# Optimization experiments

Measured on AMD Instinct MI355X. Metric: run time of the kernel, lower is better.

The kernel has to match this reference:

```python
import jax, jax.numpy as jnp
import numpy as np

NEG_SLOPE = 0.2


def add_self_loops(edge_index, num_nodes):
    loop = jnp.arange(num_nodes, dtype=edge_index.dtype)
    return jnp.concatenate([edge_index, jnp.stack([loop, loop])], axis=1)


def gat_conv(x, edge_index, W, att_src, att_dst, bias, heads, out_ch, concat):
    # x: [N, F_in]; edge_index: [2, E]; W: [F_in, heads*out_ch]
    # att_src/att_dst: [heads, out_ch]; bias: [heads*out_ch] or [out_ch]
    N = x.shape[0]
    ei = add_self_loops(edge_index, N)
    src, dst = ei[0], ei[1]
    xw = (x @ W).reshape(N, heads, out_ch)          # [N, H, C]
    a_src = jnp.einsum('nhc,hc->nh', xw, att_src)    # [N, H]
    a_dst = jnp.einsum('nhc,hc->nh', xw, att_dst)    # [N, H]
    e = a_src[src] + a_dst[dst]                      # [E', H]
    e = jax.nn.leaky_relu(e, NEG_SLOPE)
    # segment softmax over edges grouped by destination node
    e_max = jax.ops.segment_max(e, dst, num_segments=N)  # [N, H]
    e_exp = jnp.exp(e - e_max[dst])
    denom = jax.ops.segment_sum(e_exp, dst, num_segments=N)  # [N, H]
    alpha = e_exp / denom[dst]                       # [E', H]
    msg = xw[src] * alpha[:, :, None]                # [E', H, C]
    out = jax.ops.segment_sum(msg, dst, num_segments=N)  # [N, H, C]
    if concat:
        out = out.reshape(N, heads * out_ch)
    else:
        out = out.mean(axis=1)
    return out + bias


def setup_inputs() -> dict:
    key = jax.random.key(0)
    ks = jax.random.split(key, 10)
    N, E = 100000, 1600000
    F_in, hid, heads, F_out = 128, 32, 4, 40
    s = 0.1
    x = jax.random.normal(ks[0], (N, F_in), dtype=jnp.float32)
    edge_index = jax.random.randint(ks[1], (2, E), 0, N, dtype=jnp.int64)
    W1 = jax.random.normal(ks[2], (F_in, heads * hid), dtype=jnp.float32) * s
    att_src1 = jax.random.normal(ks[3], (heads, hid), dtype=jnp.float32) * s
    att_dst1 = jax.random.normal(ks[4], (heads, hid), dtype=jnp.float32) * s
    b1 = jax.random.normal(ks[5], (heads * hid,), dtype=jnp.float32) * s
    W2 = jax.random.normal(ks[6], (heads * hid, F_out), dtype=jnp.float32) * s
    att_src2 = jax.random.normal(ks[7], (1, F_out), dtype=jnp.float32) * s
    att_dst2 = jax.random.normal(ks[8], (1, F_out), dtype=jnp.float32) * s
    b2 = jax.random.normal(ks[9], (F_out,), dtype=jnp.float32) * s
    return {"x": x, "edge_index": edge_index, "W1": W1, "att_src1": att_src1,
            "att_dst1": att_dst1, "b1": b1, "W2": W2, "att_src2": att_src2,
            "att_dst2": att_dst2, "b2": b2}


def reference(x, edge_index, W1, att_src1, att_dst1, b1, W2, att_src2, att_dst2, b2):
    h = gat_conv(x, edge_index, W1, att_src1, att_dst1, b1, heads=4, out_ch=32, concat=True)
    h = jax.nn.relu(h)
    out = gat_conv(h, edge_index, W2, att_src2, att_dst2, b2, heads=1, out_ch=40, concat=True)
    return out
```

## Files before the change

kernel.cpp:

```cpp
#include <hip/hip_runtime.h>
#include <hip/hip_bf16.h>

#define NEG_SLOPE 0.2f
#define LOG2E 1.4426950408889634f
#define HWREG_XCC_ID_FULL (((32 - 1) << 11) | (0 << 6) | 20)

typedef _Float16 f16;
typedef f16 f16x8 __attribute__((ext_vector_type(8)));
typedef float f32x4 __attribute__((ext_vector_type(4)));

__device__ __forceinline__ unsigned pack_h2(float a, float b) {
    union { f16 h[2]; unsigned u; } c;
    c.h[0] = (f16)a; c.h[1] = (f16)b;
    return c.u;
}

__global__ void k_init(const int* __restrict__ ei32, int npairs, int* __restrict__ flag,
                       const float* __restrict__ W1, const float* __restrict__ W2,
                       f16* __restrict__ W1t, f16* __restrict__ W2t,
                       uint4* __restrict__ deg_part4, int nzero) {
    const int b = blockIdx.x, t = threadIdx.x;
    if (b == 0) {
        __shared__ int found;
        if (t == 0) found = 0;
        __syncthreads();
        for (int i = t; i < npairs; i += 256) {
            if (ei32[2 * i + 1] != 0) found = 1;
        }
        __syncthreads();
        if (t == 0) *flag = found ? 0 : 1;
    } else if (b <= 88) {
        int o = (b - 1) * 256 + t;
        if (o < 128 * 128) {
            int n = o >> 7, k = o & 127;
            W1t[o] = (f16)W1[k * 128 + n];
        } else {
            int o2 = o - 128 * 128;
            if (o2 < 48 * 128) {
                int n = o2 >> 7, k = o2 & 127;
                W2t[o2] = (f16)(n < 40 ? W2[k * 40 + n] : 0.f);
            }
        }
    } else {
        int idx = (b - 89) * 256 + t;
        if (idx < nzero) deg_part4[idx] = (uint4){0, 0, 0, 0};
    }
}

__global__ __launch_bounds__(1024) void k_scan_blk(int* __restrict__ deg_part,
                                                   int* __restrict__ offsets,
                                                   int* __restrict__ blksum, int N) {
    __shared__ int wsums[16];
    const int t = threadIdx.x;
    const int lane = t & 63;
    const int wid = t >> 6;
    int idx = blockIdx.x * 4096 + t * 4;
    int v0 = 0, v1 = 0, v2 = 0, v3 = 0;
    if (((N & 3) == 0) && (idx + 3 < N)) {
        uint4 u[8];
#pragma unroll
        for (int x = 0; x < 8; x++) u[x] = *(uint4*)&deg_part[x * N + idx];
        int p0 = 0, p1 = 0, p2 = 0, p3 = 0;
#pragma unroll
        for (int x = 0; x < 8; x++) {
            uint4 w = u[x];
            u[x] = (uint4){(unsigned)p0, (unsigned)p1, (unsigned)p2, (unsigned)p3};
            p0 += (int)w.x; p1 += (int)w.y; p2 += (int)w.z; p3 += (int)w.w;
        }
#pragma unroll
        for (int x = 0; x < 8; x++) *(uint4*)&deg_part[x * N + idx] = u[x];
        v0 = p0; v1 = p1; v2 = p2; v3 = p3;
    } else if (idx < N) {
        int vv[4] = {0, 0, 0, 0};
        for (int i = 0; i < 4; i++) {
            int d = idx + i;
            if (d >= N) break;
            int p = 0;
#pragma unroll
            for (int x = 0; x < 8; x++) {
                int t0 = deg_part[x * N + d];
                deg_part[x * N + d] = p;
                p += t0;
            }
            vv[i] = p;
        }
        v0 = vv[0]; v1 = vv[1]; v2 = vv[2]; v3 = vv[3];
    }
    int s1 = v0 + v1, s2 = s1 + v2, s3 = s2 + v3;
    int inc = s3;
#pragma unroll
    for (int off = 1; off < 64; off <<= 1) {
        int y = __shfl_up(inc, off);
        if (lane >= off) inc += y;
    }
    if (lane == 63) wsums[wid] = inc;
    __syncthreads();
    if (wid == 0) {
        int v = (lane < 16) ? wsums[lane] : 0;
        int wi = v;
#pragma unroll
        for (int off = 1; off < 16; off <<= 1) {
            int y = __shfl_up(wi, off);
            if (lane >= off) wi += y;
        }
        if (lane < 16) wsums[lane] = wi - v;
        if (lane == 15) blksum[blockIdx.x] = wi;
    }
    __syncthreads();
    int excl = wsums[wid] + (inc - s3);
    if (idx + 0 < N) offsets[idx + 1] = excl + v0;
    if (idx + 1 < N) offsets[idx + 2] = excl + s1;
    if (idx + 2 < N) offsets[idx + 3] = excl + s2;
    if (idx + 3 < N) offsets[idx + 4] = excl + s3;
}

__global__ void k_scan_top(const int* __restrict__ blksum, int* __restrict__ blkoff, int G) {
    int l = threadIdx.x;
    int v = (l < G) ? blksum[l] : 0;
    int inc = v;
#pragma unroll
    for (int off = 1; off < 64; off <<= 1) {
        int y = __shfl_up(inc, off);
        if (l >= off) inc += y;
    }
    if (l < G) blkoff[l] = inc - v;
}

__global__ void k_scan_add(int* __restrict__ offsets, const int* __restrict__ blkoff, int N) {
    int n = blockIdx.x * blockDim.x + threadIdx.x;
    if (n >= N) return;
    offsets[n + 1] += blkoff[n >> 12];
    if (n == 0) offsets[0] = 0;
}

__global__ void k_scatter(const void* __restrict__ ei, const int* __restrict__ flag,
                          const int* __restrict__ offsets, const int* __restrict__ deg_part,
                          const int* __restrict__ rank, int* __restrict__ csr_src,
                          int N, int E) {
    int e = blockIdx.x * blockDim.x + threadIdx.x;
    if (e >= E) return;
    int s, d;
    if (*flag) {
        const long long* p = (const long long*)ei;
        s = (int)p[e];
        d = (int)p[(long long)E + e];
    } else {
        const int* p = (const int*)ei;
        s = p[e];
        d = p[E + e];
    }
    int r = rank[e];
    int xcc = r >> 24;
    int lr = r & 0xFFFFFF;
    csr_src[offsets[d] + deg_part[xcc * N + d] + lr] = s;
}

__global__ __launch_bounds__(256) void k_gemm1deg(const float* __restrict__ X,
                                                  const f16* __restrict__ W1t,
                                                  const float* __restrict__ as1,
                                                  const float* __restrict__ ad1,
                                                  f16* __restrict__ Af,
                                                  float* __restrict__ aS1,
                                                  float* __restrict__ aD1, int N, int gb,
                                                  const void* __restrict__ ei,
                                                  const int* __restrict__ flag,
                                                  int* __restrict__ deg_part,
                                                  int* __restrict__ rank, int E) {
    __shared__ f16 sA[64 * 136];
    __shared__ f16 sB[128 * 136];
    const int t = threadIdx.x;

    if (blockIdx.x >= gb) {
        const int base = (blockIdx.x - gb) * 1024;
        const int f64 = *flag;
        const int xcc = (int)(__builtin_amdgcn_s_getreg(HWREG_XCC_ID_FULL) & 7u);
#pragma unroll
        for (int k = 0; k < 4; k++) {
            int e = base + k * 256 + t;
            if (e < E) {
                int d;
                if (f64) d = (int)((const long long*)ei)[(long long)E + e];
                else     d = ((const int*)ei)[E + e];
                int lr = atomicAdd(&deg_part[xcc * N + d], 1);
                rank[e] = (xcc << 24) | lr;
            }
        }
        return;
    }

    const int row0 = blockIdx.x * 64;
    {
        int r = t >> 2, seg = t & 3;
        int row = row0 + r;
        if (row >= N) row = N - 1;
        const float4* xg = (const float4*)(X + (size_t)row * 128 + seg * 32);
        unsigned tmp[16];
#pragma unroll
        for (int j = 0; j < 8; j++) {
            float4 v = xg[j];
            tmp[2 * j]     = pack_h2(v.x, v.y);
            tmp[2 * j + 1] = pack_h2(v.z, v.w);
        }
        uint4* dst = (uint4*)&sA[r * 136 + seg * 32];
#pragma unroll
        for (int j = 0; j < 4; j++) dst[j] = ((uint4*)tmp)[j];
        int n = t >> 1, half = (t & 1) * 64;
        const uint4* src = (const uint4*)(W1t + n * 128 + half);
        uint4* dw = (uint4*)&sB[n * 136 + half];
#pragma unroll
        for (int j = 0; j < 8; j++) dw[j] = src[j];
    }
    __syncthreads();

    const int w = t >> 6, lane = t & 63, ln = lane & 15, q = lane >> 4;
    f32x4 acc[8];
#pragma unroll
    for (int c = 0; c < 8; c++) acc[c] = (f32x4){0.f, 0.f, 0.f, 0.f};

#pragma unroll
    for (int ks = 0; ks < 4; ks++) {
        f16x8 a = *(const f16x8*)&sA[(w * 16 + ln) * 136 + ks * 32 + q * 8];
#pragma unroll
        for (int c = 0; c < 8; c++) {
            f16x8 b = *(const f16x8*)&sB[(c * 16 + ln) * 136 + ks * 32 + q * 8];
            acc[c] = __builtin_amdgcn_mfma_f32_16x16x32_f16(a, b, acc[c], 0, 0, 0);
        }
    }

#pragma unroll
    for (int c = 0; c < 8; c++)
#pragma unroll
        for (int reg = 0; reg < 4; reg++) {
            int rg = row0 + w * 16 + q * 4 + reg;
            if (rg < N) Af[(size_t)rg * 128 + c * 16 + ln] = (f16)acc[c][reg];
        }

    float ps[4][4], pd[4][4];
#pragma unroll
    for (int h = 0; h < 4; h++) {
        float as_lo = as1[32 * h + ln], as_hi = as1[32 * h + 16 + ln];
        float ad_lo = ad1[32 * h + ln], ad_hi = ad1[32 * h + 16 + ln];
#pragma unroll
        for (int reg = 0; reg < 4; reg++) {
            ps[h][reg] = acc[2 * h][reg] * as_lo + acc[2 * h + 1][reg] * as_hi;
            pd[h][reg] = acc[2 * h][reg] * ad_lo + acc[2 * h + 1][reg] * ad_hi;
        }
    }
#pragma unroll
    for (int h = 0; h < 4; h++)
#pragma unroll
        for (int reg = 0; reg < 4; reg++)
#pragma unroll
            for (int off = 1; off < 16; off <<= 1) {
                ps[h][reg] += __shfl_xor(ps[h][reg], off);
                pd[h][reg] += __shfl_xor(pd[h][reg], off);
            }
#pragma unroll
    for (int h = 0; h < 4; h++) {
        if (ln == 2 * h) {
#pragma unroll
            for (int reg = 0; reg < 4; reg++) {
                int rg = row0 + w * 16 + q * 4 + reg;
                if (rg < N) aS1[rg * 4 + h] = ps[h][reg] * LOG2E;
            }
        }
        if (ln == 2 * h + 1) {
#pragma unroll
            for (int reg = 0; reg < 4; reg++) {
                int rg = row0 + w * 16 + q * 4 + reg;
                if (rg < N) aD1[rg * 4 + h] = pd[h][reg] * LOG2E;
            }
        }
    }
}

__global__ __launch_bounds__(256) void k_gemm2(const f16* __restrict__ Hf,
                                               const f16* __restrict__ W2t,
                                               const float* __restrict__ as2,
                                               const float* __restrict__ ad2,
                                               f16* __restrict__ X2f,
                                               float* __restrict__ aS2,
                                               float* __restrict__ aD2, int N) {
    __shared__ f16 sA[64 * 136];
    __shared__ f16 sB[48 * 136];
    const int t = threadIdx.x;
    const int row0 = blockIdx.x * 64;
    {
        int r = t >> 2, seg = t & 3;
        int row = row0 + r;
        if (row >= N) row = N - 1;
        const uint4* hg = (const uint4*)(Hf + (size_t)row * 128 + seg * 32);
        uint4* dst = (uint4*)&sA[r * 136 + seg * 32];
#pragma unroll
        for (int j = 0; j < 4; j++) dst[j] = hg[j];
        const uint4* wsrc = (const uint4*)W2t;
#pragma unroll
        for (int u = t; u < 768; u += 256) {
            int o = u * 8;
            int n = o >> 7, ko = o & 127;
            *(uint4*)&sB[n * 136 + ko] = wsrc[u];
        }
    }
    __syncthreads();

    const int w = t >> 6, lane = t & 63, ln = lane & 15, q = lane >> 4;
    f32x4 acc[3];
#pragma unroll
    for (int c = 0; c < 3; c++) acc[c] = (f32x4){0.f, 0.f, 0.f, 0.f};

#pragma unroll
    for (int ks = 0; ks < 4; ks++) {
        f16x8 a = *(const f16x8*)&sA[(w * 16 + ln) * 136 + ks * 32 + q * 8];
#pragma unroll
        for (int c = 0; c < 3; c++) {
            f16x8 b = *(const f16x8*)&sB[(c * 16 + ln) * 136 + ks * 32 + q * 8];
            acc[c] = __builtin_amdgcn_mfma_f32_16x16x32_f16(a, b, acc[c], 0, 0, 0);
        }
    }

#pragma unroll
    for (int c = 0; c < 3; c++) {
        int col = c * 16 + ln;
        if (col < 40) {
#pragma unroll
            for (int reg = 0; reg < 4; reg++) {
                int rg = row0 + w * 16 + q * 4 + reg;
                if (rg < N) X2f[(size_t)rg * 64 + col] = (f16)acc[c][reg];
            }
        }
    }

    float ps[4], pd[4];
#pragma unroll
    for (int reg = 0; reg < 4; reg++) { ps[reg] = 0.f; pd[reg] = 0.f; }
#pragma unroll
    for (int c = 0; c < 3; c++) {
        int col = c * 16 + ln;
        float as_ = (col < 40) ? as2[col] : 0.f;
        float ad_ = (col < 40) ? ad2[col] : 0.f;
#pragma unroll
        for (int reg = 0; reg < 4; reg++) {
            ps[reg] = fmaf(acc[c][reg], as_, ps[reg]);
            pd[reg] = fmaf(acc[c][reg], ad_, pd[reg]);
        }
    }
#pragma unroll
    for (int reg = 0; reg < 4; reg++) {
#pragma unroll
        for (int off = 1; off < 16; off <<= 1) {
            ps[reg] += __shfl_xor(ps[reg], off);
            pd[reg] += __shfl_xor(pd[reg], off);
        }
        int rg = row0 + w * 16 + q * 4 + reg;
        if (rg < N) {
            if (ln == 0) aS2[rg] = ps[reg] * LOG2E;
            if (ln == 1) aD2[rg] = pd[reg] * LOG2E;
        }
    }
}

__global__ __launch_bounds__(256) void k_msg1(const int* __restrict__ offsets,
                                              const int* __restrict__ csr_src,
                                              const float* __restrict__ aS,
                                              const float* __restrict__ aD,
                                              const f16* __restrict__ Af,
                                              const float* __restrict__ b1,
                                              f16* __restrict__ Hf, int N) {
    const int lane = threadIdx.x & 63;
    const int n = blockIdx.x * 4 + (threadIdx.x >> 6);
    const bool node_ok = (n < N);
    const int g = lane >> 4;
    const int p = lane & 15;
    const int h = p >> 2;

    int b = 0, e = 0;
    float adh = 0.f;
    if (node_ok) {
        b = offsets[n];
        e = offsets[n + 1];
        adh = aD[n * 4 + h];
    }

    float acc[8];
#pragma unroll
    for (int k = 0; k < 8; k++) acc[k] = 0.f;
    float wsum = 0.f;

    if (node_ok) {
        float xs = aS[n * 4 + h] + adh;
        float ws = __builtin_amdgcn_exp2f(fmaxf(xs, NEG_SLOPE * xs));
        if (g != 0) ws = 0.f;
        const f16x8 hv = *(const f16x8*)(Af + (size_t)n * 128 + p * 8);
#pragma unroll
        for (int k = 0; k < 8; k++) acc[k] = fmaf(ws, (float)hv[k], acc[k]);
        wsum = ws;
    }

    int sreg = 0;
    if (node_ok && e > b) {
        int idx = b + lane;
        if (idx >= e) idx = e - 1;
        sreg = csr_src[idx];
    }

    int i = b;
#pragma unroll 2
    for (; i < e && (i - b) + 4 <= 64; i += 4) {
        int j = i + g;
        bool valid = (j < e);
        int s = __builtin_amdgcn_ds_bpermute((j - b) << 2, sreg);
        if (!valid) s = 0;
        float sv = aS[s * 4 + h];
        const f16x8 hv = *(const f16x8*)(Af + (size_t)s * 128 + p * 8);
        float x = sv + adh;
        float wgt = __builtin_amdgcn_exp2f(fmaxf(x, NEG_SLOPE * x));
        if (!valid) wgt = 0.f;
#pragma unroll
        for (int k = 0; k < 8; k++) acc[k] = fmaf(wgt, (float)hv[k], acc[k]);
        wsum += wgt;
    }
    for (; i < e; i += 4) {
        int j = i + g;
        bool valid = (j < e);
        int jc = valid ? j : (e - 1);
        int s = csr_src[jc];
        if (!valid) s = 0;
        float sv = aS[s * 4 + h];
        const f16x8 hv = *(const f16x8*)(Af + (size_t)s * 128 + p * 8);
        float x = sv + adh;
        float wgt = __builtin_amdgcn_exp2f(fmaxf(x, NEG_SLOPE * x));
        if (!valid) wgt = 0.f;
#pragma unroll
        for (int k = 0; k < 8; k++) acc[k] = fmaf(wgt, (float)hv[k], acc[k]);
        wsum += wgt;
    }

#pragma unroll
    for (int k = 0; k < 8; k++) {
        acc[k] += __shfl_xor(acc[k], 16);
        acc[k] += __shfl_xor(acc[k], 32);
    }
    wsum += __shfl_xor(wsum, 16);
    wsum += __shfl_xor(wsum, 32);

    if (node_ok && g == 0) {
        float inv = __builtin_amdgcn_rcpf(wsum);
        const float4* bb = (const float4*)(b1 + p * 8);
        float4 b0 = bb[0], b4 = bb[1];
        float bv[8] = {b0.x, b0.y, b0.z, b0.w, b4.x, b4.y, b4.z, b4.w};
        union { f16 h8[8]; uint4 u; } o;
#pragma unroll
        for (int k = 0; k < 8; k++) {
            float v = fmaf(acc[k], inv, bv[k]);
            o.h8[k] = (f16)fmaxf(v, 0.f);
        }
        *(uint4*)(Hf + (size_t)n * 128 + p * 8) = o.u;
    }
}

__global__ __launch_bounds__(256) void k_msg2(const int* __restrict__ offsets,
                                              const int* __restrict__ csr_src,
                                              const float* __restrict__ aS,
                                              const float* __restrict__ aD,
                                              const f16* __restrict__ X2f,
                                              const float* __restrict__ b2,
                                              float* __restrict__ OUT, int N) {
    __shared__ float red[4][60][9];
    const int lane = threadIdx.x & 63;
    const int wv = threadIdx.x >> 6;
    const int n = blockIdx.x * 4 + wv;
    const bool node_ok = (n < N);
    const int g = lane / 5;
    const int p = lane % 5;
    const bool lane_ok = (g < 12);

    int b = 0, e = 0;
    float adh = 0.f;
    if (node_ok) {
        b = offsets[n];
        e = offsets[n + 1];
        adh = aD[n];
    }

    float acc[8];
#pragma unroll
    for (int k = 0; k < 8; k++) acc[k] = 0.f;
    float wsum = 0.f;

    if (node_ok) {
        float xs = aS[n] + adh;
        float ws = __builtin_amdgcn_exp2f(fmaxf(xs, NEG_SLOPE * xs));
        if (!(lane_ok && g == 0)) ws = 0.f;
        const f16x8 hv = *(const f16x8*)(X2f + (size_t)n * 64 + p * 8);
#pragma unroll
        for (int k = 0; k < 8; k++) acc[k] = fmaf(ws, (float)hv[k], acc[k]);
        wsum = ws;
    }

    int sreg = 0;
    if (node_ok && e > b) {
        int idx = b + lane;
        if (idx >= e) idx = e - 1;
        sreg = csr_src[idx];
    }

    int i = b;
    for (; i < e && (i - b) + 12 <= 64; i += 12) {
        int j = i + g;
        bool valid = lane_ok && (j < e);
        int s = __builtin_amdgcn_ds_bpermute(((j - b) & 63) << 2, sreg);
        if (!valid) s = 0;
        float sv = aS[s];
        const f16x8 hv = *(const f16x8*)(X2f + (size_t)s * 64 + p * 8);
        float x = sv + adh;
        float wgt = __builtin_amdgcn_exp2f(fmaxf(x, NEG_SLOPE * x));
        if (!valid) wgt = 0.f;
#pragma unroll
        for (int k = 0; k < 8; k++) acc[k] = fmaf(wgt, (float)hv[k], acc[k]);
        wsum += wgt;
    }
    for (; i < e; i += 12) {
        int j = i + g;
        bool valid = lane_ok && (j < e);
        int jc = (j < e) ? j : (e - 1);
        int s = csr_src[jc];
        if (!valid) s = 0;
        float sv = aS[s];
        const f16x8 hv = *(const f16x8*)(X2f + (size_t)s * 64 + p * 8);
        float x = sv + adh;
        float wgt = __builtin_amdgcn_exp2f(fmaxf(x, NEG_SLOPE * x));
        if (!valid) wgt = 0.f;
#pragma unroll
        for (int k = 0; k < 8; k++) acc[k] = fmaf(wgt, (float)hv[k], acc[k]);
        wsum += wgt;
    }

    if (lane_ok) {
#pragma unroll
        for (int k = 0; k < 8; k++) red[wv][lane][k] = acc[k];
        red[wv][lane][8] = wsum;
    }
    __syncthreads();

    if (node_ok && lane < 40) {
        int pp = lane >> 3, kk = lane & 7;
        float s_ = 0.f, ws_ = 0.f;
#pragma unroll
        for (int gg = 0; gg < 12; gg++) {
            s_  += red[wv][gg * 5 + pp][kk];
            ws_ += red[wv][gg * 5][8];
        }
        float inv = __builtin_amdgcn_rcpf(ws_);
        OUT[(size_t)n * 40 + lane] = fmaf(s_, inv, b2[lane]);
    }
}

extern "C" void kernel_launch(void* const* d_in, const int* in_sizes, int n_in,
                              void* d_out, int out_size, void* d_ws, size_t ws_size,
                              hipStream_t stream) {
    const float* x   = (const float*)d_in[0];
    const void*  ei  = d_in[1];
    const float* W1  = (const float*)d_in[2];
    const float* as1 = (const float*)d_in[3];
    const float* ad1 = (const float*)d_in[4];
    const float* b1  = (const float*)d_in[5];
    const float* W2  = (const float*)d_in[6];
    const float* as2 = (const float*)d_in[7];
    const float* ad2 = (const float*)d_in[8];
    const float* b2  = (const float*)d_in[9];
    float* out = (float*)d_out;

    const int N = in_sizes[0] / 128;
    const int E = in_sizes[1] / 2;

    char* w = (char*)d_ws;
    auto alloc = [&](size_t bytes) {
        char* p = w;
        w += (bytes + 15) & ~(size_t)15;
        return p;
    };
    int* flag      = (int*)alloc(16);
    int* offsets   = (int*)alloc((size_t)(N + 1) * 4);
    int* deg_part  = (int*)alloc((size_t)N * 8 * 4);
    int* rank      = (int*)alloc((size_t)E * 4);
    int* csr_src   = (int*)alloc((size_t)E * 4);
    int* blksum    = (int*)alloc(64 * 4);
    int* blkoff    = (int*)alloc(64 * 4);
    float* aS1     = (float*)alloc((size_t)N * 4 * 4);
    float* aD1     = (float*)alloc((size_t)N * 4 * 4);
    float* aS2     = (float*)alloc((size_t)N * 4);
    float* aD2     = (float*)alloc((size_t)N * 4);
    f16* W1t       = (f16*)alloc(128 * 128 * 2);
    f16* W2t       = (f16*)alloc(48 * 128 * 2);
    f16* Af        = (f16*)alloc((size_t)N * 128 * 2);
    f16* X2f       = (f16*)alloc((size_t)N * 64 * 2);
    f16* Hf        = (f16*)alloc((size_t)N * 128 * 2);

    const int nzero = 2 * N;
    k_init<<<89 + (nzero + 255) / 256, 256, 0, stream>>>(
        (const int*)ei, 1024, flag, W1, W2, W1t, W2t, (uint4*)deg_part, nzero);

    const int gb = (N + 63) / 64;
    const int degB = (E + 1023) / 1024;
    k_gemm1deg<<<gb + degB, 256, 0, stream>>>(x, W1t, as1, ad1, Af, aS1, aD1, N, gb,
                                              ei, flag, deg_part, rank, E);

    const int G = (N + 4095) / 4096;
    k_scan_blk<<<G, 1024, 0, stream>>>(deg_part, offsets, blksum, N);
    k_scan_top<<<1, 64, 0, stream>>>(blksum, blkoff, G);
    k_scan_add<<<(N + 255) / 256, 256, 0, stream>>>(offsets, blkoff, N);
    k_scatter<<<(E + 255) / 256, 256, 0, stream>>>(ei, flag, offsets, deg_part, rank,
                                                   csr_src, N, E);

    k_msg1<<<(N + 3) / 4, 256, 0, stream>>>(offsets, csr_src, aS1, aD1, Af, b1, Hf, N);

    k_gemm2<<<gb, 256, 0, stream>>>(Hf, W2t, as2, ad2, X2f, aS2, aD2, N);
    k_msg2<<<(N + 3) / 4, 256, 0, stream>>>(offsets, csr_src, aS2, aD2, X2f, b2, out, N);
}
```

Before: 391.3 us.

## Split degree counting from GEMM1, pack edge metadata, shuffle-reduce layer-2 aggregation

Moves the atomic degree counting out of the fused GEMM1 kernel into its own kernel that handles four edges per thread. That kernel packs destination, XCC id and local rank into one 32-bit word, so the scatter no longer re-reads the destination column. The layer-2 message kernel switches from 12 groups of 5 lanes with an LDS reduction to 8 groups of 8 lanes reduced through cross-lane shuffles with vectorised output stores. GEMM2 now zero-fills the padded X2f columns so those lanes read valid zeros. The packing keeps only 12 bits for the local rank and 17 for the node id, which limits per-XCC in-degree and N, and GEMM1 no longer overlaps with the degree atomics.

New measurement: 395.2 us. About the same (+1.0%).

```diff
diff --git a/kernel.cpp b/kernel.cpp
--- a/kernel.cpp
+++ b/kernel.cpp
@@ -47,6 +47,34 @@
     }
 }
 
+__global__ void k_degree(const void* __restrict__ ei, const int* __restrict__ flag,
+                         int* __restrict__ deg_part, unsigned* __restrict__ packed,
+                         int N, int E) {
+    const int base = (blockIdx.x * blockDim.x + threadIdx.x) * 4;
+    if (base >= E) return;
+    const int f64 = *flag;
+    const int xcc = (int)(__builtin_amdgcn_s_getreg(HWREG_XCC_ID_FULL) & 7u);
+    int dv[4];
+    if (f64) {
+        const long long* p = (const long long*)ei + E;
+#pragma unroll
+        for (int k = 0; k < 4; k++) dv[k] = (base + k < E) ? (int)p[base + k] : 0;
+    } else {
+        const int* p = (const int*)ei + E;
+#pragma unroll
+        for (int k = 0; k < 4; k++) dv[k] = (base + k < E) ? p[base + k] : 0;
+    }
+    unsigned pk[4];
+#pragma unroll
+    for (int k = 0; k < 4; k++) {
+        int lr = (base + k < E) ? atomicAdd(&deg_part[xcc * N + dv[k]], 1) : 0;
+        pk[k] = ((unsigned)dv[k] << 15) | ((unsigned)xcc << 12) | (unsigned)lr;
+    }
+#pragma unroll
+    for (int k = 0; k < 4; k++)
+        if (base + k < E) packed[base + k] = pk[k];
+}
+
 __global__ __launch_bounds__(1024) void k_scan_blk(int* __restrict__ deg_part,
                                                    int* __restrict__ offsets,
                                                    int* __restrict__ blksum, int N) {
@@ -135,60 +163,48 @@
 
 __global__ void k_scatter(const void* __restrict__ ei, const int* __restrict__ flag,
                           const int* __restrict__ offsets, const int* __restrict__ deg_part,
-                          const int* __restrict__ rank, int* __restrict__ csr_src,
+                          const unsigned* __restrict__ packed, int* __restrict__ csr_src,
                           int N, int E) {
-    int e = blockIdx.x * blockDim.x + threadIdx.x;
-    if (e >= E) return;
-    int s, d;
-    if (*flag) {
+    const int base = (blockIdx.x * blockDim.x + threadIdx.x) * 4;
+    if (base >= E) return;
+    const int f64 = *flag;
+    int sv[4];
+    if (f64) {
         const long long* p = (const long long*)ei;
-        s = (int)p[e];
-        d = (int)p[(long long)E + e];
+#pragma unroll
+        for (int k = 0; k < 4; k++) sv[k] = (base + k < E) ? (int)p[base + k] : 0;
     } else {
         const int* p = (const int*)ei;
-        s = p[e];
-        d = p[E + e];
-    }
-    int r = rank[e];
-    int xcc = r >> 24;
-    int lr = r & 0xFFFFFF;
-    csr_src[offsets[d] + deg_part[xcc * N + d] + lr] = s;
-}
-
-__global__ __launch_bounds__(256) void k_gemm1deg(const float* __restrict__ X,
-                                                  const f16* __restrict__ W1t,
-                                                  const float* __restrict__ as1,
-                                                  const float* __restrict__ ad1,
-                                                  f16* __restrict__ Af,
-                                                  float* __restrict__ aS1,
-                                                  float* __restrict__ aD1, int N, int gb,
-                                                  const void* __restrict__ ei,
-                                                  const int* __restrict__ flag,
-                                                  int* __restrict__ deg_part,
-                                                  int* __restrict__ rank, int E) {
+#pragma unroll
+        for (int k = 0; k < 4; k++) sv[k] = (base + k < E) ? p[base + k] : 0;
+    }
+    unsigned pk[4];
+#pragma unroll
+    for (int k = 0; k < 4; k++) pk[k] = (base + k < E) ? packed[base + k] : 0;
+#pragma unroll
+    for (int k = 0; k < 4; k++) {
+        if (base + k < E) {
+            unsigned u = pk[k];
+            int d = (int)(u >> 15);
+            int xcc = (int)((u >> 12) & 7u);
+            int lr = (int)(u & 0xFFFu);
+            csr_src[offsets[d] + deg_part[xcc * N + d] + lr] = sv[k];
+        }
+    }
+}
+
+__global__ __launch_bounds__(256) void k_gemm1(const float* __restrict__ X,
+                                               const f16* __restrict__ W1t,
+                                               const float* __restrict__ as1,
+                                               const float* __restrict__ ad1,
+                                               f16* __restrict__ Af,
+                                               float* __restrict__ aS1,
+                                               float* __restrict__ aD1, int N) {
     __shared__ f16 sA[64 * 136];
     __shared__ f16 sB[128 * 136];
     const int t = threadIdx.x;
-
-    if (blockIdx.x >= gb) {
-        const int base = (blockIdx.x - gb) * 1024;
-        const int f64 = *flag;
-        const int xcc = (int)(__builtin_amdgcn_s_getreg(HWREG_XCC_ID_FULL) & 7u);
-#pragma unroll
-        for (int k = 0; k < 4; k++) {
-            int e = base + k * 256 + t;
-            if (e < E) {
-                int d;
-                if (f64) d = (int)((const long long*)ei)[(long long)E + e];
-                else     d = ((const int*)ei)[E + e];
-                int lr = atomicAdd(&deg_part[xcc * N + d], 1);
-                rank[e] = (xcc << 24) | lr;
-            }
-        }
-        return;
-    }
-
     const int row0 = blockIdx.x * 64;
+
     {
         int r = t >> 2, seg = t & 3;
         int row = row0 + r;
@@ -327,6 +343,20 @@
                 int rg = row0 + w * 16 + q * 4 + reg;
                 if (rg < N) X2f[(size_t)rg * 64 + col] = (f16)acc[c][reg];
             }
+        } else {
+#pragma unroll
+            for (int reg = 0; reg < 4; reg++) {
+                int rg = row0 + w * 16 + q * 4 + reg;
+                if (rg < N) X2f[(size_t)rg * 64 + col] = (f16)0.f;
+            }
+        }
+    }
+    {
+        int col = 48 + ln;
+#pragma unroll
+        for (int reg = 0; reg < 4; reg++) {
+            int rg = row0 + w * 16 + q * 4 + reg;
+            if (rg < N) X2f[(size_t)rg * 64 + col] = (f16)0.f;
         }
     }
 
@@ -465,14 +495,11 @@
                                               const f16* __restrict__ X2f,
                                               const float* __restrict__ b2,
                                               float* __restrict__ OUT, int N) {
-    __shared__ float red[4][60][9];
     const int lane = threadIdx.x & 63;
-    const int wv = threadIdx.x >> 6;
-    const int n = blockIdx.x * 4 + wv;
+    const int n = blockIdx.x * 4 + (threadIdx.x >> 6);
     const bool node_ok = (n < N);
-    const int g = lane / 5;
-    const int p = lane % 5;
-    const bool lane_ok = (g < 12);
+    const int g = lane >> 3;
+    const int p = lane & 7;
 
     int b = 0, e = 0;
     float adh = 0.f;
@@ -490,7 +517,7 @@
     if (node_ok) {
         float xs = aS[n] + adh;
         float ws = __builtin_amdgcn_exp2f(fmaxf(xs, NEG_SLOPE * xs));
-        if (!(lane_ok && g == 0)) ws = 0.f;
+        if (g != 0) ws = 0.f;
         const f16x8 hv = *(const f16x8*)(X2f + (size_t)n * 64 + p * 8);
 #pragma unroll
         for (int k = 0; k < 8; k++) acc[k] = fmaf(ws, (float)hv[k], acc[k]);
@@ -505,10 +532,11 @@
     }
 
     int i = b;
-    for (; i < e && (i - b) + 12 <= 64; i += 12) {
+#pragma unroll 2
+    for (; i < e && (i - b) + 8 <= 64; i += 8) {
         int j = i + g;
-        bool valid = lane_ok && (j < e);
-        int s = __builtin_amdgcn_ds_bpermute(((j - b) & 63) << 2, sreg);
+        bool valid = (j < e);
+        int s = __builtin_amdgcn_ds_bpermute((j - b) << 2, sreg);
         if (!valid) s = 0;
         float sv = aS[s];
         const f16x8 hv = *(const f16x8*)(X2f + (size_t)s * 64 + p * 8);
@@ -519,10 +547,10 @@
         for (int k = 0; k < 8; k++) acc[k] = fmaf(wgt, (float)hv[k], acc[k]);
         wsum += wgt;
     }
-    for (; i < e; i += 12) {
+    for (; i < e; i += 8) {
         int j = i + g;
-        bool valid = lane_ok && (j < e);
-        int jc = (j < e) ? j : (e - 1);
+        bool valid = (j < e);
+        int jc = valid ? j : (e - 1);
         int s = csr_src[jc];
         if (!valid) s = 0;
         float sv = aS[s];
@@ -535,23 +563,29 @@
         wsum += wgt;
     }
 
-    if (lane_ok) {
-#pragma unroll
-        for (int k = 0; k < 8; k++) red[wv][lane][k] = acc[k];
-        red[wv][lane][8] = wsum;
-    }
-    __syncthreads();
-
-    if (node_ok && lane < 40) {
-        int pp = lane >> 3, kk = lane & 7;
-        float s_ = 0.f, ws_ = 0.f;
-#pragma unroll
-        for (int gg = 0; gg < 12; gg++) {
-            s_  += red[wv][gg * 5 + pp][kk];
-            ws_ += red[wv][gg * 5][8];
-        }
-        float inv = __builtin_amdgcn_rcpf(ws_);
-        OUT[(size_t)n * 40 + lane] = fmaf(s_, inv, b2[lane]);
+#pragma unroll
+    for (int k = 0; k < 8; k++) {
+        acc[k] += __shfl_xor(acc[k], 8);
+        acc[k] += __shfl_xor(acc[k], 16);
+        acc[k] += __shfl_xor(acc[k], 32);
+    }
+    wsum += __shfl_xor(wsum, 8);
+    wsum += __shfl_xor(wsum, 16);
+    wsum += __shfl_xor(wsum, 32);
+
+    if (node_ok && g == 0 && p < 5) {
+        float inv = __builtin_amdgcn_rcpf(wsum);
+        const float4* bb = (const float4*)(b2 + p * 8);
+        float4 b0 = bb[0], b4 = bb[1];
+        float bv[8] = {b0.x, b0.y, b0.z, b0.w, b4.x, b4.y, b4.z, b4.w};
+        float4 o0, o1;
+        o0.x = fmaf(acc[0], inv, bv[0]); o0.y = fmaf(acc[1], inv, bv[1]);
+        o0.z = fmaf(acc[2], inv, bv[2]); o0.w = fmaf(acc[3], inv, bv[3]);
+        o1.x = fmaf(acc[4], inv, bv[4]); o1.y = fmaf(acc[5], inv, bv[5]);
+        o1.z = fmaf(acc[6], inv, bv[6]); o1.w = fmaf(acc[7], inv, bv[7]);
+        float* op = OUT + (size_t)n * 40 + p * 8;
+        *(float4*)op = o0;
+        *(float4*)(op + 4) = o1;
     }
 }
 
@@ -579,39 +613,37 @@
         w += (bytes + 15) & ~(size_t)15;
         return p;
     };
-    int* flag      = (int*)alloc(16);
-    int* offsets   = (int*)alloc((size_t)(N + 1) * 4);
-    int* deg_part  = (int*)alloc((size_t)N * 8 * 4);
-    int* rank      = (int*)alloc((size_t)E * 4);
-    int* csr_src   = (int*)alloc((size_t)E * 4);
-    int* blksum    = (int*)alloc(64 * 4);
-    int* blkoff    = (int*)alloc(64 * 4);
-    float* aS1     = (float*)alloc((size_t)N * 4 * 4);
-    float* aD1     = (float*)alloc((size_t)N * 4 * 4);
-    float* aS2     = (float*)alloc((size_t)N * 4);
-    float* aD2     = (float*)alloc((size_t)N * 4);
-    f16* W1t       = (f16*)alloc(128 * 128 * 2);
-    f16* W2t       = (f16*)alloc(48 * 128 * 2);
-    f16* Af        = (f16*)alloc((size_t)N * 128 * 2);
-    f16* X2f       = (f16*)alloc((size_t)N * 64 * 2);
-    f16* Hf        = (f16*)alloc((size_t)N * 128 * 2);
+    int* flag        = (int*)alloc(16);
+    int* offsets     = (int*)alloc((size_t)(N + 1) * 4);
+    int* deg_part    = (int*)alloc((size_t)N * 8 * 4);
+    unsigned* packed = (unsigned*)alloc((size_t)E * 4);
+    int* csr_src     = (int*)alloc((size_t)E * 4);
+    int* blksum      = (int*)alloc(64 * 4);
+    int* blkoff      = (int*)alloc(64 * 4);
+    float* aS1       = (float*)alloc((size_t)N * 4 * 4);
+    float* aD1       = (float*)alloc((size_t)N * 4 * 4);
+    float* aS2       = (float*)alloc((size_t)N * 4);
+    float* aD2       = (float*)alloc((size_t)N * 4);
+    f16* W1t         = (f16*)alloc(128 * 128 * 2);
+    f16* W2t         = (f16*)alloc(48 * 128 * 2);
+    f16* Af          = (f16*)alloc((size_t)N * 128 * 2);
+    f16* X2f         = (f16*)alloc((size_t)N * 64 * 2);
+    f16* Hf          = (f16*)alloc((size_t)N * 128 * 2);
 
     const int nzero = 2 * N;
     k_init<<<89 + (nzero + 255) / 256, 256, 0, stream>>>(
         (const int*)ei, 1024, flag, W1, W2, W1t, W2t, (uint4*)deg_part, nzero);
 
-    const int gb = (N + 63) / 64;
-    const int degB = (E + 1023) / 1024;
-    k_gemm1deg<<<gb + degB, 256, 0, stream>>>(x, W1t, as1, ad1, Af, aS1, aD1, N, gb,
-                                              ei, flag, deg_part, rank, E);
-
+    k_degree<<<(E + 1023) / 1024, 256, 0, stream>>>(ei, flag, deg_part, packed, N, E);
     const int G = (N + 4095) / 4096;
     k_scan_blk<<<G, 1024, 0, stream>>>(deg_part, offsets, blksum, N);
     k_scan_top<<<1, 64, 0, stream>>>(blksum, blkoff, G);
     k_scan_add<<<(N + 255) / 256, 256, 0, stream>>>(offsets, blkoff, N);
-    k_scatter<<<(E + 255) / 256, 256, 0, stream>>>(ei, flag, offsets, deg_part, rank,
-                                                   csr_src, N, E);
-
+    k_scatter<<<(E + 1023) / 1024, 256, 0, stream>>>(ei, flag, offsets, deg_part,
+                                                     packed, csr_src, N, E);
+
+    const int gb = (N + 63) / 64;
+    k_gemm1<<<gb, 256, 0, stream>>>(x, W1t, as1, ad1, Af, aS1, aD1, N);
     k_msg1<<<(N + 3) / 4, 256, 0, stream>>>(offsets, csr_src, aS1, aD1, Af, b1, Hf, N);
 
     k_gemm2<<<gb, 256, 0, stream>>>(Hf, W2t, as2, ad2, X2f, aS2, aD2, N);
```
